# Kernel tuning notes

Hardware: AMD Instinct MI355X
Metric: run time of the kernel (lower is better)

## Reference

```python
import jax, jax.numpy as jnp
import numpy as np

NUM_FIELDS = 10
VOCAB = 100000
EMBED_DIM = 8
BATCH = 16384

def setup_inputs() -> dict:
    key = jax.random.key(0)
    k1, k2, k3 = jax.random.split(key, 3)
    x = jax.random.randint(k1, (BATCH, NUM_FIELDS), 0, VOCAB)  # categorical ids per field
    # field-aware embedding tables: V[i, j, v, :] = embedding of feature v in field i
    # used when interacting with field j  (xavier-ish small init)
    V = jax.random.normal(k2, (NUM_FIELDS, NUM_FIELDS, VOCAB, EMBED_DIM), dtype=jnp.float32) * 0.01
    # linear (first-order) weights, one scalar per feature id per field
    L = jax.random.normal(k3, (NUM_FIELDS, VOCAB), dtype=jnp.float32) * 0.01
    bias = jnp.zeros((), dtype=jnp.float32)
    return {"x": x, "bias": bias, "L": L, "V": V}

def reference(x, bias, L, V):
    B, F = x.shape
    idx = jnp.arange(F)
    xt = x.T  # (F, B)
    # first-order term: sum_i L[i, x[:, i]] -> (B,)
    first = L[idx[:, None], xt].sum(axis=0)
    # field-aware gather: E[i, j, b, :] = V[i, j, x[b, i], :]  -> (F, F, B, D)
    E = V[idx[:, None, None], idx[None, :, None], xt[:, None, :]]
    # pairwise interactions: P[i, j, b] = <V[i][j](x_i), V[j][i](x_j)>
    P = jnp.einsum('ijbd,jibd->ijb', E, E)
    mask = jnp.triu(jnp.ones((F, F), dtype=bool), k=1)  # i < j only
    second = jnp.where(mask[:, :, None], P, 0.0).sum(axis=(0, 1))  # (B,)
    logit = bias + first + second
    return jax.nn.sigmoid(logit)[:, None]  # (B, 1)
```

## Files before the change

### kernel.cpp

```cpp
#include <hip/hip_runtime.h>
#include <math.h>

#define NFIELDS 10
#define VOCAB   100000
#define EDIM    8
#define BATCH   16384
#define NPAIR   45

__global__ __launch_bounds__(256) void ffm_kernel(
    const int*   __restrict__ x,
    const float* __restrict__ bias,
    const float* __restrict__ L,
    const float* __restrict__ V,
    float*       __restrict__ out)
{
    const int lane = threadIdx.x & 63;
    const int wave = threadIdx.x >> 6;
    const int b    = blockIdx.x * 4 + wave;

    float acc = 0.0f;

    if (lane < NPAIR) {
        int p = lane;
        int i = 0;
        int cnt = NFIELDS - 1;
        while (p >= cnt) { p -= cnt; ++i; --cnt; }
        const int j = i + 1 + p;

        const int xi = x[b * NFIELDS + i];
        const int xj = x[b * NFIELDS + j];

        const float* va = V + (((size_t)i * NFIELDS + j) * VOCAB + (size_t)xi) * EDIM;
        const float* vb = V + (((size_t)j * NFIELDS + i) * VOCAB + (size_t)xj) * EDIM;

        const float4 a0 = ((const float4*)va)[0];
        const float4 a1 = ((const float4*)va)[1];
        const float4 b0 = ((const float4*)vb)[0];
        const float4 b1 = ((const float4*)vb)[1];

        acc = a0.x * b0.x + a0.y * b0.y + a0.z * b0.z + a0.w * b0.w
            + a1.x * b1.x + a1.y * b1.y + a1.z * b1.z + a1.w * b1.w;
    } else if (lane < NPAIR + NFIELDS) {
        const int i  = lane - NPAIR;
        const int xi = x[b * NFIELDS + i];
        acc = L[(size_t)i * VOCAB + (size_t)xi];
    }

    #pragma unroll
    for (int off = 32; off > 0; off >>= 1)
        acc += __shfl_down(acc, off, 64);

    if (lane == 0) {
        const float logit = acc + bias[0];
        out[b] = 1.0f / (1.0f + expf(-logit));
    }
}

extern "C" void kernel_launch(void* const* d_in, const int* in_sizes, int n_in,
                              void* d_out, int out_size, void* d_ws, size_t ws_size,
                              hipStream_t stream) {
    const int*   x    = (const int*)  d_in[0];
    const float* bias = (const float*)d_in[1];
    const float* L    = (const float*)d_in[2];
    const float* V    = (const float*)d_in[3];
    float*       out  = (float*)d_out;

    const int blocks = BATCH / 4;
    ffm_kernel<<<blocks, 256, 0, stream>>>(x, bias, L, V, out);
}
```

Measured before the change: 390.8 us.

## Split FFM into per-pair gather kernel and separate reduction kernel

Replaces the one-wave-per-sample kernel with two kernels. The first uses a grid over (batch tiles, pair) so each block gathers a single (i,j) table pair for 256 samples and writes the dot products to a workspace. The second sums the 45 partial results plus the linear terms per sample and applies the sigmoid. Restricting each block to one table pair is meant to improve locality of the random gathers. It costs an extra launch and a 45xBATCH workspace round trip, and it relies on d_ws being large enough.

```diff
diff --git a/kernel.cpp b/kernel.cpp
--- a/kernel.cpp
+++ b/kernel.cpp
@@ -7,53 +7,54 @@
 #define BATCH   16384
 #define NPAIR   45
 
-__global__ __launch_bounds__(256) void ffm_kernel(
+__global__ __launch_bounds__(256) void ffm_pairs(
+    const int*   __restrict__ x,
+    const float* __restrict__ V,
+    float*       __restrict__ P)
+{
+    const int p = blockIdx.y;
+    int i = 0, rem = p, cnt = NFIELDS - 1;
+    while (rem >= cnt) { rem -= cnt; ++i; --cnt; }
+    const int j = i + 1 + rem;
+
+    const int b  = blockIdx.x * 256 + threadIdx.x;
+    const int xi = x[b * NFIELDS + i];
+    const int xj = x[b * NFIELDS + j];
+
+    const float4* va = (const float4*)(V + (((size_t)i * NFIELDS + j) * VOCAB + (size_t)xi) * EDIM);
+    const float4* vb = (const float4*)(V + (((size_t)j * NFIELDS + i) * VOCAB + (size_t)xj) * EDIM);
+
+    const float4 a0 = va[0];
+    const float4 a1 = va[1];
+    const float4 b0 = vb[0];
+    const float4 b1 = vb[1];
+
+    const float dot = a0.x * b0.x + a0.y * b0.y + a0.z * b0.z + a0.w * b0.w
+                    + a1.x * b1.x + a1.y * b1.y + a1.z * b1.z + a1.w * b1.w;
+
+    P[(size_t)p * BATCH + b] = dot;
+}
+
+__global__ __launch_bounds__(256) void ffm_reduce(
     const int*   __restrict__ x,
     const float* __restrict__ bias,
     const float* __restrict__ L,
-    const float* __restrict__ V,
+    const float* __restrict__ P,
     float*       __restrict__ out)
 {
-    const int lane = threadIdx.x & 63;
-    const int wave = threadIdx.x >> 6;
-    const int b    = blockIdx.x * 4 + wave;
+    const int b = blockIdx.x * 256 + threadIdx.x;
 
-    float acc = 0.0f;
-
-    if (lane < NPAIR) {
-        int p = lane;
-        int i = 0;
-        int cnt = NFIELDS - 1;
-        while (p >= cnt) { p -= cnt; ++i; --cnt; }
-        const int j = i + 1 + p;
-
-        const int xi = x[b * NFIELDS + i];
-        const int xj = x[b * NFIELDS + j];
-
-        const float* va = V + (((size_t)i * NFIELDS + j) * VOCAB + (size_t)xi) * EDIM;
-        const float* vb = V + (((size_t)j * NFIELDS + i) * VOCAB + (size_t)xj) * EDIM;
-
-        const float4 a0 = ((const float4*)va)[0];
-        const float4 a1 = ((const float4*)va)[1];
-        const float4 b0 = ((const float4*)vb)[0];
-        const float4 b1 = ((const float4*)vb)[1];
-
-        acc = a0.x * b0.x + a0.y * b0.y + a0.z * b0.z + a0.w * b0.w
-            + a1.x * b1.x + a1.y * b1.y + a1.z * b1.z + a1.w * b1.w;
-    } else if (lane < NPAIR + NFIELDS) {
-        const int i  = lane - NPAIR;
-        const int xi = x[b * NFIELDS + i];
-        acc = L[(size_t)i * VOCAB + (size_t)xi];
-    }
+    float s = bias[0];
 
     #pragma unroll
-    for (int off = 32; off > 0; off >>= 1)
-        acc += __shfl_down(acc, off, 64);
+    for (int p = 0; p < NPAIR; ++p)
+        s += P[(size_t)p * BATCH + b];
 
-    if (lane == 0) {
-        const float logit = acc + bias[0];
-        out[b] = 1.0f / (1.0f + expf(-logit));
-    }
+    #pragma unroll
+    for (int i = 0; i < NFIELDS; ++i)
+        s += L[(size_t)i * VOCAB + (size_t)x[b * NFIELDS + i]];
+
+    out[b] = 1.0f / (1.0f + expf(-s));
 }
 
 extern "C" void kernel_launch(void* const* d_in, const int* in_sizes, int n_in,
@@ -64,7 +65,9 @@
     const float* L    = (const float*)d_in[2];
     const float* V    = (const float*)d_in[3];
     float*       out  = (float*)d_out;
+    float*       P    = (float*)d_ws;
 
-    const int blocks = BATCH / 4;
-    ffm_kernel<<<blocks, 256, 0, stream>>>(x, bias, L, V, out);
+    dim3 gridA(BATCH / 256, NPAIR);
+    ffm_pairs<<<gridA, 256, 0, stream>>>(x, V, P);
+    ffm_reduce<<<BATCH / 256, 256, 0, stream>>>(x, bias, L, P, out);
 }
```

New measurement: 399.4 us. +2.2%, slower.
